# Optimization experiments

Measured on AMD Instinct MI355X. Metric: run time of the kernel, lower is better.

The kernel has to match this reference:

```python
import jax, jax.numpy as jnp
import numpy as np

IMG_W, IMG_H = 640, 360
STRIDE = 32
S = 72                      # n_offsets
FMAP_H, FMAP_W = IMG_H // STRIDE, IMG_W // STRIDE   # 11, 20
CF = 64                     # anchor_feat_channels
CBACK = 512                 # resnet34 output channels
NP = 4                      # n_proposal
B = 512
F = CF * FMAP_H             # 704


def setup_inputs() -> dict:
    key = jax.random.key(0)
    ks = jax.random.split(key, 8)
    feat = jax.random.normal(ks[0], (B, CBACK, FMAP_H, FMAP_W), dtype=jnp.float32)
    # rpn proposals: (x_px, y_px, unused, angle_deg)
    x = jax.random.uniform(ks[1], (B, NP)) * IMG_W
    y = jax.random.uniform(ks[2], (B, NP)) * IMG_H
    ang = 30.0 + jax.random.uniform(ks[3], (B, NP)) * 120.0   # degrees in [30,150]
    rpn_proposals = jnp.stack([x, y, jnp.zeros_like(x), ang], axis=-1).astype(jnp.float32)
    conv_w = jax.random.normal(ks[4], (CF, CBACK), dtype=jnp.float32) * 0.02
    conv_b = jnp.zeros((CF,), jnp.float32)
    att_w = jax.random.normal(ks[5], (NP - 1, F), dtype=jnp.float32) * 0.02
    att_b = jnp.zeros((NP - 1,), jnp.float32)
    cls_w = jax.random.normal(ks[6], (2, 2 * F), dtype=jnp.float32) * 0.02
    cls_b = jnp.zeros((2,), jnp.float32)
    reg_w = jax.random.normal(ks[7], (S + 1, 2 * F), dtype=jnp.float32) * 0.02
    reg_b = jnp.zeros((S + 1,), jnp.float32)
    return {"feat": feat, "rpn_proposals": rpn_proposals, "conv_w": conv_w,
            "conv_b": conv_b, "att_w": att_w, "att_b": att_b,
            "cls_w": cls_w, "cls_b": cls_b, "reg_w": reg_w, "reg_b": reg_b}


# off-diagonal scatter pattern of the 4x4 attention matrix (row-major order of eye==0)
_ROWS = np.repeat(np.arange(NP), NP - 1)                       # (12,)
_COLS = np.array([j for i in range(NP) for j in range(NP) if j != i])  # (12,)


def reference(feat, rpn_proposals, conv_w, conv_b, att_w, att_b, cls_w, cls_b, reg_w, reg_b):
    bsz = feat.shape[0]
    anchor_ys = jnp.linspace(1.0, 0.0, S)          # (72,)
    anchor_cut_ys = jnp.linspace(1.0, 0.0, FMAP_H) # (11,)

    # --- generate_anchor (vectorized over batch x 4 proposals) ---
    start_x = rpn_proposals[..., 0] / IMG_W        # (B,4)
    start_y = rpn_proposals[..., 1] / IMG_H        # (B,4)
    tan = jnp.tan(rpn_proposals[..., 3] * (np.pi / 180.0))
    xs_full = (start_x[..., None] + (start_y[..., None] - anchor_ys) / tan[..., None]) * IMG_W      # (B,4,72)
    xs_cut = (start_x[..., None] + (start_y[..., None] - anchor_cut_ys) / tan[..., None]) * IMG_W   # (B,4,11)

    anchors = jnp.zeros((bsz, NP, 5 + S), jnp.float32)
    anchors = anchors.at[..., 2].set(1.0 - start_y)
    anchors = anchors.at[..., 3].set(start_x)
    anchors = anchors.at[..., 5:].set(xs_full)

    # --- anchor cut indices (flip along fmap_h like the original) ---
    unclamped = jnp.flip(jnp.round(xs_cut / STRIDE).astype(jnp.int32), axis=-1)  # (B,4,11)
    cut_x = jnp.clip(unclamped, 0, FMAP_W - 1)
    invalid = (unclamped < 0) | (unclamped > FMAP_W)   # faithful: > fmap_w, not >=

    # --- conv1 (1x1 conv) ---
    f = jnp.einsum('bchw,oc->bohw', feat, conv_w) + conv_b[None, :, None, None]  # (B,64,11,20)

    # --- cut_anchor_features: gather f[b, c, y, cut_x[b,p,y]], zero invalid ---
    g = jnp.take_along_axis(f[:, None], cut_x[:, :, None, :, None], axis=4)[..., 0]  # (B,4,64,11)
    g = jnp.where(invalid[:, :, None, :], 0.0, g)
    anchor_feat = g.reshape(bsz, NP, F)  # (B,4,704)

    # --- attention: softmax over 3 non-self anchors, scattered off-diagonal ---
    scores = anchor_feat.reshape(-1, F) @ att_w.T + att_b          # (B*4,3)
    attention = jax.nn.softmax(scores, axis=1).reshape(bsz, NP, NP - 1)
    att_mat = jnp.zeros((bsz, NP, NP), jnp.float32).at[:, _ROWS, _COLS].set(attention.reshape(bsz, -1))

    # attention_features[b,i,:] = sum_j att_mat[b,i,j] * anchor_feat[b,j,:]
    att_feat = jnp.einsum('bij,bjf->bif', att_mat, anchor_feat)    # (B,4,704)
    cat = jnp.concatenate([att_feat, anchor_feat], axis=-1)        # (B,4,1408)

    cls_logits = cat @ cls_w.T + cls_b                             # (B,4,2)
    reg = cat @ reg_w.T + reg_b                                    # (B,4,73)

    reg_proposals = anchors
    reg_proposals = reg_proposals.at[..., :2].set(cls_logits)
    reg_proposals = reg_proposals.at[..., 4:].add(reg)
    # nms(): with conf_threshold=None, anchors[:,:,0]==0 so num_to_keep==4 -> all kept.
    return reg_proposals
```

## Files before the change

### kernel.cpp

```cpp
#include <hip/hip_runtime.h>
#include <math.h>

#define NPROP 4
#define SFULL 72
#define FH 11
#define FW 20
#define CB 512
#define FDIM 704
#define HW 220
#define CHT 32
#define NTILE 16
#define MROWS 160

typedef __attribute__((ext_vector_type(8))) short bf16x8;
typedef __attribute__((ext_vector_type(4))) float f32x4;

__device__ __forceinline__ unsigned short f2bf(float x) {
  unsigned u = __float_as_uint(x);
  u += 0x7FFFu + ((u >> 16) & 1u);
  return (unsigned short)(u >> 16);
}
__device__ __forceinline__ unsigned bfbits(float x) {
  unsigned u = __float_as_uint(x);
  return u + 0x7FFFu + ((u >> 16) & 1u);
}

__device__ __forceinline__ void gload16(const void* g, void* l) {
  __builtin_amdgcn_global_load_lds(
      (const __attribute__((address_space(1))) void*)(g),
      (__attribute__((address_space(3))) void*)(l), 16, 0, 0);
}

__global__ void k_prep(const float* __restrict__ cls_w, const float* __restrict__ reg_w,
                       const float* __restrict__ att_w, const float* __restrict__ conv_w,
                       unsigned short* __restrict__ Wc, unsigned short* __restrict__ Wb2) {
  const int blk = blockIdx.x;
  const int t = threadIdx.x;
  if (blk < MROWS) {
    const int m = blk;
    const float* rowp = nullptr;
    if (m < 150) {
      int o = (m < 75) ? m : m - 75;
      int half = (m < 75) ? 0 : FDIM;
      rowp = ((o < 2) ? (cls_w + o * 2 * FDIM) : (reg_w + (o - 2) * 2 * FDIM)) + half;
    } else if (m < 153) {
      rowp = att_w + (m - 150) * FDIM;
    }
    for (int f = t; f < FDIM; f += 256) {
      float v = rowp ? rowp[f] : 0.0f;
      int fp = (f % FH) * 64 + (f / FH);
      Wc[m * FDIM + fp] = f2bf(v);
    }
  } else {
    const int kg = blk - MROWS;
    #pragma unroll
    for (int e0 = 0; e0 < 2; e0++) {
      int e = t + 256 * e0;
      Wb2[kg * 512 + e] = f2bf(conv_w[(e >> 3) * CB + kg * 8 + (e & 7)]);
    }
  }
}

__global__ __launch_bounds__(512, 4) void k_gconv(
    const float* __restrict__ feat, const float* __restrict__ rpn,
    const unsigned short* __restrict__ Wb2, const float* __restrict__ conv_b,
    unsigned short* __restrict__ af, float* __restrict__ xs_full,
    float* __restrict__ out)
{
  __shared__ __align__(16) unsigned short W2[64 * 512];
  __shared__ __align__(16) unsigned short As[3 * 44 * 40];
  __shared__ float sh_sx[NPROP], sh_sy[NPROP], sh_it[NPROP];
  __shared__ int   sh_pos[48];
  __shared__ int   hcnt[55];
  __shared__ unsigned hword[55];

  const int b = blockIdx.x;
  const int t = threadIdx.x;
  const int l = t & 63;
  const int wid = t >> 6;
  const int nt = wid & 3;
  const int mhalf = wid >> 2;
  const int q = l >> 4, r = l & 15;

  if (t < NPROP) {
    const float* rp = rpn + (b * NPROP + t) * 4;
    float sx = rp[0] * (1.0f / 640.0f);
    float sy = rp[1] * (1.0f / 360.0f);
    float tn = tanf(rp[3] * 0.017453292519943295f);
    sh_sx[t] = sx; sh_sy[t] = sy; sh_it[t] = 1.0f / tn;
    out[(b * NPROP + t) * 77 + 2] = 1.0f - sy;
    out[(b * NPROP + t) * 77 + 3] = sx;
  }
  __syncthreads();
  if (t < NPROP * SFULL) {
    int p = t / SFULL, i = t - p * SFULL;
    float ay = 1.0f - (float)i * (1.0f / 71.0f);
    xs_full[(b * NPROP + p) * SFULL + i] =
        (sh_sx[p] + (sh_sy[p] - ay) * sh_it[p]) * 640.0f;
  }
  if (t < 48) {
    int ps = -1;
    if (t < NPROP * FH) {
      int p = t / FH, y = t - p * FH;
      float acy = 1.0f - (float)(10 - y) * 0.1f;
      float xc = (sh_sx[p] + (sh_sy[p] - acy) * sh_it[p]) * 640.0f;
      int ui = (int)rintf(xc * (1.0f / 32.0f));
      int cut = min(max(ui, 0), FW - 1);
      ps = ((ui < 0) | (ui > FW)) ? -1 : (t % FH) * FW + cut;
    }
    sh_pos[t] = ps;
  }
  __syncthreads();

  if (t < 55) {
    int cnt = 0; unsigned w = 0;
    for (int s = 0; s < 44; s++) {
      int p = sh_pos[s];
      if (p >= 0 && (p >> 2) == t) {
        w |= ((unsigned)(s | ((p & 3) << 6))) << (8 * cnt);
        cnt++;
      }
    }
    hcnt[t] = cnt; hword[t] = w;
  }
  __syncthreads();

  int hn[4]; unsigned hwd[4]; int chS[4]; int cid[4];
  const int cbase = 220 * wid;
  #pragma unroll
  for (int k = 0; k < 4; k++) {
    int c = cbase + 64 * k + l;
    bool ok = (k < 3) || (l < 28);
    cid[k] = c;
    int j = c % 55;
    chS[k] = c / 55;
    hn[k]  = ok ? hcnt[j] : 0;
    hwd[k] = hword[j];
  }

  const float* fb = feat + (size_t)b * (CB * HW);

  #pragma unroll
  for (int k = 0; k < 8; k++) {
    int chunk = t + 512 * k;
    gload16(Wb2 + chunk * 8, (void*)&W2[chunk * 8]);
  }
  __builtin_amdgcn_sched_barrier(0);

  float4 pf[3][4];
  #pragma unroll
  for (int s = 0; s < 3; s++) {
    const float4* g = (const float4*)(fb + s * (CHT * HW));
    #pragma unroll
    for (int k = 0; k < 3; k++) pf[s][k] = g[cid[k]];
    if (l < 28) pf[s][3] = g[cid[3]];
    __builtin_amdgcn_sched_barrier(0);
  }

  f32x4 acc0 = {0.f, 0.f, 0.f, 0.f}, acc1 = {0.f, 0.f, 0.f, 0.f};
  const int cW = 16 * nt + r;

#define MFMA_STEP(pt) { \
    const unsigned short* Asp = As + ((pt) % 3) * 1760; \
    bf16x8 bw = *(const bf16x8*)&W2[(((pt) * 4 + q) * 64 + cW) * 8]; \
    if (mhalf == 0) { \
      bf16x8 a0 = *(const bf16x8*)&Asp[(0 + r) * 40 + q * 8]; \
      bf16x8 a1 = *(const bf16x8*)&Asp[(16 + r) * 40 + q * 8]; \
      asm volatile("s_waitcnt lgkmcnt(0)" ::: "memory"); \
      __builtin_amdgcn_sched_barrier(0); \
      acc0 = __builtin_amdgcn_mfma_f32_16x16x32_bf16(a0, bw, acc0, 0, 0, 0); \
      acc1 = __builtin_amdgcn_mfma_f32_16x16x32_bf16(a1, bw, acc1, 0, 0, 0); \
    } else { \
      bf16x8 a2 = *(const bf16x8*)&Asp[(32 + r) * 40 + q * 8]; \
      asm volatile("s_waitcnt lgkmcnt(0)" ::: "memory"); \
      __builtin_amdgcn_sched_barrier(0); \
      acc0 = __builtin_amdgcn_mfma_f32_16x16x32_bf16(a2, bw, acc0, 0, 0, 0); \
    } }

  #pragma unroll
  for (int ct = 0; ct < NTILE; ct++) {
    if (ct <= 13)      asm volatile("s_waitcnt vmcnt(8)" ::: "memory");
    else if (ct == 14) asm volatile("s_waitcnt vmcnt(4)" ::: "memory");
    else               asm volatile("s_waitcnt vmcnt(0)" ::: "memory");
    __builtin_amdgcn_sched_barrier(0);

    unsigned short* Asb = As + (ct % 3) * 1760;
    #pragma unroll
    for (int k = 0; k < 4; k++) {
      int n = hn[k];
      if (n) {
        float4 v4 = pf[ct % 3][k];
        unsigned d0 = (bfbits(v4.x) >> 16) | (bfbits(v4.y) & 0xFFFF0000u);
        unsigned d1 = (bfbits(v4.z) >> 16) | (bfbits(v4.w) & 0xFFFF0000u);
        unsigned wd = hwd[k];
        #pragma unroll
        for (int h = 0; h < 4; h++) {
          if (h < n) {
            unsigned byte = (wd >> (8 * h)) & 255u;
            unsigned s = byte & 63u;
            unsigned sel = (byte & 128u) ? d1 : d0;
            unsigned short val = (byte & 64u) ? (unsigned short)(sel >> 16)
                                              : (unsigned short)sel;
            Asb[s * 40 + chS[k]] = val;
          }
        }
      }
    }
    if (ct + 3 < NTILE) {
      const float4* g = (const float4*)(fb + (ct + 3) * (CHT * HW));
      #pragma unroll
      for (int k = 0; k < 3; k++) pf[ct % 3][k] = g[cid[k]];
      if (l < 28) pf[ct % 3][3] = g[cid[3]];
    }
    asm volatile("s_waitcnt lgkmcnt(0)" ::: "memory");
    __builtin_amdgcn_sched_barrier(0);
    __builtin_amdgcn_s_barrier();
    __builtin_amdgcn_sched_barrier(0);

    if (ct > 0) MFMA_STEP(ct - 1)
  }
  MFMA_STEP(15)
#undef MFMA_STEP

  {
    const int c = cW;
    const int g = q;
    const float cb = conv_b[c];
    #pragma unroll
    for (int rr = 0; rr < 4; rr++) {
      if (mhalf == 0) {
        int m0 = g * 4 + rr;
        int p = m0 / FH, y = m0 - p * FH;
        float v = (sh_pos[m0] >= 0) ? (acc0[rr] + cb) : 0.0f;
        af[(size_t)(b * NPROP + p) * FDIM + y * 64 + c] = f2bf(v);
        int m1 = 16 + g * 4 + rr;
        p = m1 / FH; y = m1 - p * FH;
        v = (sh_pos[m1] >= 0) ? (acc1[rr] + cb) : 0.0f;
        af[(size_t)(b * NPROP + p) * FDIM + y * 64 + c] = f2bf(v);
      } else {
        int m2 = 32 + g * 4 + rr;
        if (m2 < 44) {
          int p = m2 / FH, y = m2 - p * FH;
          float v = (sh_pos[m2] >= 0) ? (acc0[rr] + cb) : 0.0f;
          af[(size_t)(b * NPROP + p) * FDIM + y * 64 + c] = f2bf(v);
        }
      }
    }
  }
}

__global__ __launch_bounds__(256) void k_head(
    const unsigned short* __restrict__ af, const float* __restrict__ xs,
    const unsigned short* __restrict__ Wc,
    const float* __restrict__ att_b, const float* __restrict__ cls_b,
    const float* __restrict__ reg_b, float* __restrict__ out)
{
  __shared__ __align__(16) unsigned short A_s[16 * 712];
  __shared__ __align__(16) unsigned short W_s[2][MROWS * 40];
  __shared__ float Ys[16 * 161];
  __shared__ float Am[16][4];

  const int bg = blockIdx.x;
  const int t = threadIdx.x;
  const int l = t & 63;
  const int wid = t >> 6;

  {
    const unsigned* src = (const unsigned*)af + (size_t)bg * 16 * 352;
    for (int i = t; i < 16 * 352; i += 256) {
      int r = i / 352, ci = i - r * 352;
      ((unsigned*)A_s)[r * 356 + ci] = src[i];
    }
  }
  {
    #pragma unroll
    for (int e = t; e < 640; e += 256) {
      int n = e >> 2, jj = e & 3;
      uint4 ld = *(const uint4*)(Wc + n * FDIM + jj * 8);
      *(uint4*)(&W_s[0][n * 40 + jj * 8]) = ld;
    }
  }
  __syncthreads();

  f32x4 acc[3];
  acc[0] = (f32x4){0.f,0.f,0.f,0.f}; acc[1] = acc[0]; acc[2] = acc[0];

  for (int step = 0; step < 22; ++step) {
    int cur = step & 1;
    uint4 r0, r1, r2;
    bool h2 = (t + 512) < 640;
    if (step < 21) {
      int k0 = (step + 1) * 32;
      { int e = t;       int n = e >> 2, jj = e & 3; r0 = *(const uint4*)(Wc + n * FDIM + k0 + jj * 8); }
      { int e = t + 256; int n = e >> 2, jj = e & 3; r1 = *(const uint4*)(Wc + n * FDIM + k0 + jj * 8); }
      if (h2) { int e = t + 512; int n = e >> 2, jj = e & 3; r2 = *(const uint4*)(Wc + n * FDIM + k0 + jj * 8); }
    }
    bf16x8 a = *(const bf16x8*)(A_s + (l & 15) * 712 + step * 32 + (l >> 4) * 8);
    #pragma unroll
    for (int j = 0; j < 3; j++) {
      int ntl = wid + 4 * j;
      if (ntl < 10) {
        bf16x8 bb = *(const bf16x8*)(&W_s[cur][(ntl * 16 + (l & 15)) * 40 + (l >> 4) * 8]);
        acc[j] = __builtin_amdgcn_mfma_f32_16x16x32_bf16(a, bb, acc[j], 0, 0, 0);
      }
    }
    if (step < 21) {
      { int e = t;       int n = e >> 2, jj = e & 3; *(uint4*)(&W_s[cur ^ 1][n * 40 + jj * 8]) = r0; }
      { int e = t + 256; int n = e >> 2, jj = e & 3; *(uint4*)(&W_s[cur ^ 1][n * 40 + jj * 8]) = r1; }
      if (h2) { int e = t + 512; int n = e >> 2, jj = e & 3; *(uint4*)(&W_s[cur ^ 1][n * 40 + jj * 8]) = r2; }
    }
    __syncthreads();
  }

  #pragma unroll
  for (int j = 0; j < 3; j++) {
    int ntl = wid + 4 * j;
    if (ntl < 10) {
      #pragma unroll
      for (int r = 0; r < 4; r++)
        Ys[((l >> 4) * 4 + r) * 161 + ntl * 16 + (l & 15)] = acc[j][r];
    }
  }
  __syncthreads();

  if (t < 16) {
    float s0 = Ys[t * 161 + 150] + att_b[0];
    float s1 = Ys[t * 161 + 151] + att_b[1];
    float s2 = Ys[t * 161 + 152] + att_b[2];
    float mx = fmaxf(s0, fmaxf(s1, s2));
    float e0 = expf(s0 - mx), e1 = expf(s1 - mx), e2 = expf(s2 - mx);
    float inv = 1.0f / (e0 + e1 + e2);
    float aa[3] = {e0 * inv, e1 * inv, e2 * inv};
    int p = t & 3;
    #pragma unroll
    for (int qq = 0; qq < NPROP; qq++)
      Am[t][qq] = (qq == p) ? 0.0f : aa[(qq < p) ? qq : qq - 1];
  }
  __syncthreads();

  for (int d = t; d < 16 * 75; d += 256) {
    int row = d / 75, o = d - row * 75;
    float v = Ys[row * 161 + 75 + o];
    int base = row & ~3;
    #pragma unroll
    for (int qq = 0; qq < NPROP; qq++) v += Am[row][qq] * Ys[(base + qq) * 161 + o];
    v += (o < 2) ? cls_b[o] : reg_b[o - 2];
    int grow = bg * 16 + row;
    int col = (o < 2) ? o : o + 2;
    if (o >= 3) v += xs[grow * SFULL + (o - 3)];
    out[grow * 77 + col] = v;
  }
}

extern "C" void kernel_launch(void* const* d_in, const int* in_sizes, int n_in,
                              void* d_out, int out_size, void* d_ws, size_t ws_size,
                              hipStream_t stream) {
  const float* feat   = (const float*)d_in[0];
  const float* rpn    = (const float*)d_in[1];
  const float* conv_w = (const float*)d_in[2];
  const float* conv_b = (const float*)d_in[3];
  const float* att_w  = (const float*)d_in[4];
  const float* att_b  = (const float*)d_in[5];
  const float* cls_w  = (const float*)d_in[6];
  const float* cls_b  = (const float*)d_in[7];
  const float* reg_w  = (const float*)d_in[8];
  const float* reg_b  = (const float*)d_in[9];
  float* out = (float*)d_out;

  char* ws = (char*)d_ws;
  unsigned short* af  = (unsigned short*)ws;
  float* xs           = (float*)(ws + 2883584);
  unsigned short* Wc  = (unsigned short*)(ws + 2883584 + 589824);
  unsigned short* Wb2 = (unsigned short*)(ws + 2883584 + 589824 + 225280);

  k_prep<<<224, 256, 0, stream>>>(cls_w, reg_w, att_w, conv_w, Wc, Wb2);
  k_gconv<<<512, 512, 0, stream>>>(feat, rpn, Wb2, conv_b, af, xs, out);
  k_head<<<128, 256, 0, stream>>>(af, xs, Wc, att_b, cls_b, reg_b, out);
}
```

Before: 68.75 us.

## Process two channel tiles per barrier with four-deep prefetch ring

```diff
diff --git a/kernel.cpp b/kernel.cpp
--- a/kernel.cpp
+++ b/kernel.cpp
@@ -68,7 +68,7 @@
     float* __restrict__ out)
 {
   __shared__ __align__(16) unsigned short W2[64 * 512];
-  __shared__ __align__(16) unsigned short As[3 * 44 * 40];
+  __shared__ __align__(16) unsigned short As[4 * 1760 + 160];
   __shared__ float sh_sx[NPROP], sh_sy[NPROP], sh_it[NPROP];
   __shared__ int   sh_pos[48];
   __shared__ int   hcnt[55];
@@ -147,9 +147,9 @@
   }
   __builtin_amdgcn_sched_barrier(0);
 
-  float4 pf[3][4];
-  #pragma unroll
-  for (int s = 0; s < 3; s++) {
+  float4 pf[4][4];
+  #pragma unroll
+  for (int s = 0; s < 4; s++) {
     const float4* g = (const float4*)(fb + s * (CHT * HW));
     #pragma unroll
     for (int k = 0; k < 3; k++) pf[s][k] = g[cid[k]];
@@ -160,8 +160,35 @@
   f32x4 acc0 = {0.f, 0.f, 0.f, 0.f}, acc1 = {0.f, 0.f, 0.f, 0.f};
   const int cW = 16 * nt + r;
 
+#define SCATTER(ct) { \
+    unsigned short* Asb = As + ((ct) & 3) * 1760; \
+    _Pragma("unroll") \
+    for (int k = 0; k < 4; k++) { \
+      int n = hn[k]; \
+      if (n) { \
+        float4 v4 = pf[(ct) & 3][k]; \
+        unsigned d0 = (bfbits(v4.x) >> 16) | (bfbits(v4.y) & 0xFFFF0000u); \
+        unsigned d1 = (bfbits(v4.z) >> 16) | (bfbits(v4.w) & 0xFFFF0000u); \
+        unsigned wd = hwd[k]; \
+        _Pragma("unroll") \
+        for (int h = 0; h < 4; h++) { \
+          if (h < n) { \
+            unsigned byte = (wd >> (8 * h)) & 255u; \
+            unsigned s = byte & 63u; \
+            unsigned sel = (byte & 128u) ? d1 : d0; \
+            unsigned short val = (byte & 64u) ? (unsigned short)(sel >> 16) \
+                                              : (unsigned short)sel; \
+            Asb[s * 40 + chS[k]] = val; \
+          } } } } }
+
+#define ISSUE(ct) { \
+    const float4* g = (const float4*)(fb + (ct) * (CHT * HW)); \
+    _Pragma("unroll") \
+    for (int k = 0; k < 3; k++) pf[(ct) & 3][k] = g[cid[k]]; \
+    if (l < 28) pf[(ct) & 3][3] = g[cid[3]]; }
+
 #define MFMA_STEP(pt) { \
-    const unsigned short* Asp = As + ((pt) % 3) * 1760; \
+    const unsigned short* Asp = As + ((pt) & 3) * 1760; \
     bf16x8 bw = *(const bf16x8*)&W2[(((pt) * 4 + q) * 64 + cW) * 8]; \
     if (mhalf == 0) { \
       bf16x8 a0 = *(const bf16x8*)&Asp[(0 + r) * 40 + q * 8]; \
@@ -178,48 +205,28 @@
     } }
 
   #pragma unroll
-  for (int ct = 0; ct < NTILE; ct++) {
-    if (ct <= 13)      asm volatile("s_waitcnt vmcnt(8)" ::: "memory");
-    else if (ct == 14) asm volatile("s_waitcnt vmcnt(4)" ::: "memory");
-    else               asm volatile("s_waitcnt vmcnt(0)" ::: "memory");
+  for (int pj = 0; pj < 8; pj++) {
+    if (pj <= 6) { asm volatile("s_waitcnt vmcnt(8)" ::: "memory"); }
+    else         { asm volatile("s_waitcnt vmcnt(0)" ::: "memory"); }
     __builtin_amdgcn_sched_barrier(0);
 
-    unsigned short* Asb = As + (ct % 3) * 1760;
-    #pragma unroll
-    for (int k = 0; k < 4; k++) {
-      int n = hn[k];
-      if (n) {
-        float4 v4 = pf[ct % 3][k];
-        unsigned d0 = (bfbits(v4.x) >> 16) | (bfbits(v4.y) & 0xFFFF0000u);
-        unsigned d1 = (bfbits(v4.z) >> 16) | (bfbits(v4.w) & 0xFFFF0000u);
-        unsigned wd = hwd[k];
-        #pragma unroll
-        for (int h = 0; h < 4; h++) {
-          if (h < n) {
-            unsigned byte = (wd >> (8 * h)) & 255u;
-            unsigned s = byte & 63u;
-            unsigned sel = (byte & 128u) ? d1 : d0;
-            unsigned short val = (byte & 64u) ? (unsigned short)(sel >> 16)
-                                              : (unsigned short)sel;
-            Asb[s * 40 + chS[k]] = val;
-          }
-        }
-      }
-    }
-    if (ct + 3 < NTILE) {
-      const float4* g = (const float4*)(fb + (ct + 3) * (CHT * HW));
-      #pragma unroll
-      for (int k = 0; k < 3; k++) pf[ct % 3][k] = g[cid[k]];
-      if (l < 28) pf[ct % 3][3] = g[cid[3]];
+    SCATTER(2 * pj)
+    SCATTER(2 * pj + 1)
+
+    if (pj <= 5) {
+      ISSUE(2 * pj + 4)
+      ISSUE(2 * pj + 5)
     }
     asm volatile("s_waitcnt lgkmcnt(0)" ::: "memory");
     __builtin_amdgcn_sched_barrier(0);
     __builtin_amdgcn_s_barrier();
     __builtin_amdgcn_sched_barrier(0);
 
-    if (ct > 0) MFMA_STEP(ct - 1)
-  }
-  MFMA_STEP(15)
+    MFMA_STEP(2 * pj)
+    MFMA_STEP(2 * pj + 1)
+  }
+#undef SCATTER
+#undef ISSUE
 #undef MFMA_STEP
 
   {
```

Measured after the change: 69.75 us. No clear change (+1.5%).
